# Performance work log

Measured on AMD Instinct MI355X. Metric: run time of the kernel, lower is better.

## Reference

```python
import jax, jax.numpy as jnp
import numpy as np

B, S, D, H, HD, MEM = 2, 2048, 1024, 16, 64, 512
SPARSITY_Q = 0.1


def setup_inputs() -> dict:
    key = jax.random.key(0)
    ks = jax.random.split(key, 12)
    s = 1.0 / np.sqrt(D).astype(np.float32)
    return {
        "hidden_states": jax.random.normal(ks[0], (B, S, D), jnp.float32),
        "attention_mask": jnp.ones((B, S), jnp.int32),
        "past_k": jax.random.normal(ks[1], (B, H, MEM, HD), jnp.float32),
        "past_v": jax.random.normal(ks[2], (B, H, MEM, HD), jnp.float32),
        "Wq": jax.random.normal(ks[3], (D, D), jnp.float32) * s,
        "bq": jnp.zeros((D,), jnp.float32),
        "Wk": jax.random.normal(ks[4], (D, D), jnp.float32) * s,
        "bk": jnp.zeros((D,), jnp.float32),
        "Wv": jax.random.normal(ks[5], (D, D), jnp.float32) * s,
        "bv": jnp.zeros((D,), jnp.float32),
        "Wo": jax.random.normal(ks[6], (D, D), jnp.float32) * s,
        "bo": jnp.zeros((D,), jnp.float32),
    }


def reference(hidden_states, attention_mask, past_k, past_v,
              Wq, bq, Wk, bk, Wv, bv, Wo, bo):
    b, s, d = hidden_states.shape
    # projections -> [b, h, s, hd]
    def split_heads(x):
        return x.reshape(b, s, H, HD).transpose(0, 2, 1, 3)
    q = split_heads(hidden_states @ Wq + bq)
    k = split_heads(hidden_states @ Wk + bk)
    v = split_heads(hidden_states @ Wv + bv)
    # concat KV cache along key length
    k = jnp.concatenate([past_k, k], axis=2)  # [b, h, mem+s, hd]
    v = jnp.concatenate([past_v, v], axis=2)
    past_len = past_k.shape[2]
    mask = jnp.concatenate(
        [jnp.ones((b, past_len), attention_mask.dtype), attention_mask], axis=1)
    scale = 1.0 / float(np.sqrt(HD))
    scores = jnp.einsum("bhqd,bhkd->bhqk", q, k) * scale  # [b,h,s,mem+s]
    # per-row quantile threshold sparsification (torch.quantile, linear interp)
    thr = jnp.quantile(scores, SPARSITY_Q, axis=-1, keepdims=True)
    neg_inf = jnp.float32(-jnp.inf)
    scores = jnp.where(scores < thr, neg_inf, scores)
    scores = jnp.where(mask[:, None, None, :] == 0, neg_inf, scores)
    attn = jax.nn.softmax(scores, axis=-1)  # dropout is identity in eval
    out = jnp.einsum("bhqk,bhkd->bhqd", attn, v)
    out = out.transpose(0, 2, 1, 3).reshape(b, s, d) @ Wo + bo
    new_k = k[:, :, -MEM:, :]
    new_v = v[:, :, -MEM:, :]
    return out, (new_k, new_v)
```

## Files before the change

### kernel.cpp

```cpp
#include <hip/hip_runtime.h>
#include <stdint.h>

typedef unsigned short ushort_t;
typedef __attribute__((ext_vector_type(8))) short bf16x8;
typedef __attribute__((ext_vector_type(4))) float f32x4;

#define BB 2
#define SS 2048
#define DD 1024
#define HH 16
#define HDD 64
#define MEMM 512
#define KTOT 2560
#define NKB 80
#define NROWS (BB*HH*SS)


__device__ __forceinline__ float bf2f(uint32_t u) {
    return __uint_as_float(u << 16);
}
__device__ __forceinline__ ushort_t f2bf(float f) {
    uint32_t u = __float_as_uint(f);
    uint32_t r = (u + 0x7FFFu + ((u >> 16) & 1u)) >> 16;
    return (ushort_t)r;
}
__device__ __forceinline__ uint32_t mapkey(uint32_t u) {
    return (u & 0x8000u) ? (0xFFFFu ^ u) : (u | 0x8000u);
}
__device__ __forceinline__ uint32_t unmapkey(uint32_t k) {
    return (k & 0x8000u) ? (k ^ 0x8000u) : (0xFFFFu ^ k);
}

__global__ __launch_bounds__(256) void cast_hidden_kernel(
    const float* __restrict__ h, ushort_t* __restrict__ hb)
{
    size_t i0 = ((size_t)blockIdx.x * 256 + threadIdx.x) * 16;
    ushort_t o[16];
#pragma unroll
    for (int j = 0; j < 4; ++j) {
        float4 v = *(const float4*)&h[i0 + j * 4];
        o[j * 4 + 0] = f2bf(v.x); o[j * 4 + 1] = f2bf(v.y);
        o[j * 4 + 2] = f2bf(v.z); o[j * 4 + 3] = f2bf(v.w);
    }
    *(uint4*)&hb[i0] = *(uint4*)&o[0];
    *(uint4*)&hb[i0 + 8] = *(uint4*)&o[8];
}

__global__ __launch_bounds__(256) void transw_kernel(
    const float* __restrict__ Wq, const float* __restrict__ Wk,
    const float* __restrict__ Wv, const float* __restrict__ Wo,
    ushort_t* __restrict__ WtAll)
{
    __shared__ ushort_t T[64][66];
    const int z = blockIdx.z;
    const float* W = (z == 0) ? Wq : (z == 1) ? Wk : (z == 2) ? Wv : Wo;
    ushort_t* dst = WtAll + (size_t)z * DD * DD;
    const int k0 = blockIdx.x * 64, n0 = blockIdx.y * 64;
    const int t = threadIdx.x;
    const int kk = t >> 2, c4 = (t & 3) * 16;
#pragma unroll
    for (int j = 0; j < 4; ++j) {
        float4 v = *(const float4*)&W[(size_t)(k0 + kk) * DD + n0 + c4 + j * 4];
        T[kk][c4 + j * 4 + 0] = f2bf(v.x);
        T[kk][c4 + j * 4 + 1] = f2bf(v.y);
        T[kk][c4 + j * 4 + 2] = f2bf(v.z);
        T[kk][c4 + j * 4 + 3] = f2bf(v.w);
    }
    __syncthreads();
    const int nn = t >> 2, kc = (t & 3) * 16;
    ushort_t tmp[16];
#pragma unroll
    for (int j = 0; j < 16; ++j) tmp[j] = T[kc + j][nn];
    *(uint4*)&dst[(size_t)(n0 + nn) * DD + k0 + kc] = *(uint4*)&tmp[0];
    *(uint4*)&dst[(size_t)(n0 + nn) * DD + k0 + kc + 8] = *(uint4*)&tmp[8];
}

__global__ __launch_bounds__(256) void gemm128_kernel(
    const ushort_t* __restrict__ A, const ushort_t* __restrict__ Bt, int mode,
    const float* __restrict__ bq, const float* __restrict__ bk, const float* __restrict__ bv,
    float* __restrict__ outf,
    ushort_t* __restrict__ q_bf, ushort_t* __restrict__ kbf, ushort_t* __restrict__ vbf,
    float* __restrict__ nk, float* __restrict__ nv)
{
    __shared__ __align__(16) ushort_t As[128 * 32];
    __shared__ __align__(16) ushort_t Bs[128 * 32];
    const int tid = threadIdx.x;
    const int lane = tid & 63, w = tid >> 6;
    const int wm = w >> 1, wn = w & 1;
    const int row16 = lane & 15, quad = lane >> 4;
    const int n0 = blockIdx.x * 128, m0 = blockIdx.y * 128;

    const int r0 = tid >> 2, c0 = (tid & 3) * 8;
    const int r1 = (tid + 256) >> 2, c1 = ((tid + 256) & 3) * 8;

    f32x4 acc[4][4];
#pragma unroll
    for (int i = 0; i < 4; ++i)
#pragma unroll
        for (int j = 0; j < 4; ++j) acc[i][j] = (f32x4){0.f, 0.f, 0.f, 0.f};

    for (int k0 = 0; k0 < DD; k0 += 32) {
        *(uint4*)&As[tid * 8]         = *(const uint4*)&A [(size_t)(m0 + r0) * DD + k0 + c0];
        *(uint4*)&As[(tid + 256) * 8] = *(const uint4*)&A [(size_t)(m0 + r1) * DD + k0 + c1];
        *(uint4*)&Bs[tid * 8]         = *(const uint4*)&Bt[(size_t)(n0 + r0) * DD + k0 + c0];
        *(uint4*)&Bs[(tid + 256) * 8] = *(const uint4*)&Bt[(size_t)(n0 + r1) * DD + k0 + c1];
        __syncthreads();
        bf16x8 af[4], bfr[4];
#pragma unroll
        for (int mt = 0; mt < 4; ++mt)
            af[mt] = *(const bf16x8*)&As[(wm * 64 + mt * 16 + row16) * 32 + quad * 8];
#pragma unroll
        for (int nt = 0; nt < 4; ++nt)
            bfr[nt] = *(const bf16x8*)&Bs[(wn * 64 + nt * 16 + row16) * 32 + quad * 8];
#pragma unroll
        for (int mt = 0; mt < 4; ++mt)
#pragma unroll
            for (int nt = 0; nt < 4; ++nt)
                acc[mt][nt] = __builtin_amdgcn_mfma_f32_16x16x32_bf16(
                    af[mt], bfr[nt], acc[mt][nt], 0, 0, 0);
        __syncthreads();
    }

#pragma unroll
    for (int nt = 0; nt < 4; ++nt) {
        const int nb = n0 + wn * 64 + nt * 16;
        if (mode == 0) {
#pragma unroll
            for (int mt = 0; mt < 4; ++mt) {
#pragma unroll
                for (int r = 0; r < 4; ++r) {
                    int m = m0 + wm * 64 + mt * 16 + quad * 4 + r;
                    int n = nb + row16;
                    outf[(size_t)m * DD + n] = acc[mt][nt][r] + bq[n];
                }
            }
        } else {
            const int sel = nb >> 10;
            const float* bias = (sel == 0) ? bq : (sel == 1) ? bk : bv;
#pragma unroll
            for (int mt = 0; mt < 4; ++mt) {
#pragma unroll
                for (int r = 0; r < 4; ++r) {
                    int m = m0 + wm * 64 + mt * 16 + quad * 4 + r;
                    int nn = (nb + row16) & 1023;
                    float v = acc[mt][nt][r] + bias[nn];
                    int b = m >> 11, s = m & (SS - 1);
                    int h = nn >> 6, d = nn & 63;
                    size_t bh = (size_t)b * HH + h;
                    if (sel == 0) {
                        q_bf[(bh * SS + s) * HDD + d] = f2bf(v);
                    } else {
                        ushort_t* dst = (sel == 1) ? kbf : vbf;
                        dst[(bh * KTOT + MEMM + s) * HDD + d] = f2bf(v);
                        if (s >= SS - MEMM) {
                            float* nf = (sel == 1) ? nk : nv;
                            nf[(bh * MEMM + (s - (SS - MEMM))) * HDD + d] = v;
                        }
                    }
                }
            }
        }
    }
}

__global__ __launch_bounds__(256) void cast_past_kernel(
    const float* __restrict__ pk, const float* __restrict__ pv,
    ushort_t* __restrict__ kbf, ushort_t* __restrict__ vbf)
{
    int idx = blockIdx.x * 256 + threadIdx.x;
    int bh = idx >> 15;
    int rem = idx & 32767;
    size_t dst = (size_t)bh * KTOT * HDD + rem;
    kbf[dst] = f2bf(pk[idx]);
    vbf[dst] = f2bf(pv[idx]);
}

__global__ __launch_bounds__(256) void transpose_v_kernel(
    const ushort_t* __restrict__ vbf, ushort_t* __restrict__ vt)
{
    __shared__ ushort_t T[64][72];
    const int k0 = blockIdx.x * 64;
    const int bh = blockIdx.y;
    const int t = threadIdx.x;
    const int rr = t >> 3, cc = (t & 7) * 8;
#pragma unroll
    for (int p = 0; p < 2; ++p) {
        int kk = p * 32 + rr;
        *(uint4*)&T[kk][cc] =
            *(const uint4*)(vbf + ((size_t)bh * KTOT + k0 + kk) * HDD + cc);
    }
    __syncthreads();
    const int ld = t & 63, nt = t >> 6;
    const int sr = ld & 15, q = ld >> 4;
#pragma unroll
    for (int kbl = 0; kbl < 2; ++kbl) {
        ushort_t tmp[8];
#pragma unroll
        for (int j = 0; j < 8; ++j) tmp[j] = T[kbl * 32 + q * 8 + j][nt * 16 + sr];
        *(uint4*)(vt + (((size_t)bh * NKB + (k0 >> 5) + kbl) * 4 + nt) * 512 + ld * 8)
            = *(uint4*)tmp;
    }
}

__global__ __launch_bounds__(256) void score_kernel(
    const ushort_t* __restrict__ qbf, const ushort_t* __restrict__ kbf,
    ushort_t* __restrict__ sbuf, int bh0)
{
    __shared__ __align__(16) ushort_t Ts[64][264];
    const int w = threadIdx.x >> 6, lane = threadIdx.x & 63;
    const int kt = blockIdx.x, qt = blockIdx.y;
    const int lbh = blockIdx.z, bh = bh0 + lbh;
    const int m0 = qt * 64 + w * 16;
    const int row16 = lane & 15, quad = lane >> 4;

    const ushort_t* qrow = qbf + ((size_t)bh * SS + m0 + row16) * HDD + quad * 8;
    bf16x8 a0 = *(const bf16x8*)qrow;
    bf16x8 a1 = *(const bf16x8*)(qrow + 32);
    const ushort_t* kbase = kbf + ((size_t)bh * KTOT + kt * 256 + row16) * HDD + quad * 8;

    bf16x8 b0c = *(const bf16x8*)kbase;
    bf16x8 b1c = *(const bf16x8*)(kbase + 32);
#pragma unroll
    for (int nt = 0; nt < 16; ++nt) {
        bf16x8 b0n, b1n;
        if (nt < 15) {
            const ushort_t* kr = kbase + (size_t)(nt + 1) * 16 * HDD;
            b0n = *(const bf16x8*)kr;
            b1n = *(const bf16x8*)(kr + 32);
        }
        f32x4 acc = {0.f, 0.f, 0.f, 0.f};
        acc = __builtin_amdgcn_mfma_f32_16x16x32_bf16(a0, b0c, acc, 0, 0, 0);
        acc = __builtin_amdgcn_mfma_f32_16x16x32_bf16(a1, b1c, acc, 0, 0, 0);
#pragma unroll
        for (int r = 0; r < 4; ++r)
            Ts[w * 16 + quad * 4 + r][nt * 16 + row16] = f2bf(acc[r] * 0.125f);
        b0c = b0n; b1c = b1n;
    }
    const int pnl = lbh * (SS / 16) + qt * 4 + w;
    ushort_t* dstb = sbuf + ((size_t)pnl * NKB + kt * 8) * 512 + lane * 8;
    const int c0 = (lane >> 4) * 8;
    const int rs = w * 16 + (lane & 15);
#pragma unroll
    for (int kbl = 0; kbl < 8; ++kbl)
        *(uint4*)(dstb + kbl * 512) = *(const uint4*)&Ts[rs][kbl * 32 + c0];
}

__device__ __forceinline__ uint32_t wave_iscan(uint32_t x, int lane) {
#pragma unroll
    for (int d = 1; d < 64; d <<= 1) {
        uint32_t t = __shfl_up(x, d, 64);
        if (lane >= d) x += t;
    }
    return x;
}
__device__ __forceinline__ void select_from_counts(
    const uint32_t* c, uint32_t R, int lane, uint32_t* bin_out, uint32_t* rem_out)
{
    uint32_t s = c[0] + c[1] + c[2] + c[3];
    uint32_t incl = wave_iscan(s, lane);
    uint32_t excl = incl - s;
    uint64_t bal = __ballot(incl > R);
    int fl = __ffsll((unsigned long long)bal) - 1;
    uint32_t exf = __shfl(excl, fl, 64);
    uint32_t c0 = __shfl(c[0], fl, 64), c1 = __shfl(c[1], fl, 64);
    uint32_t c2 = __shfl(c[2], fl, 64), c3 = __shfl(c[3], fl, 64);
    uint32_t cc[4] = {c0, c1, c2, c3};
    uint32_t cum = exf, bin = fl * 4, rem = 0;
#pragma unroll
    for (int i = 0; i < 4; ++i) {
        if (cum + cc[i] > R) { bin = fl * 4 + i; rem = R - cum; break; }
        cum += cc[i];
    }
    *bin_out = bin;
    *rem_out = rem;
}

__device__ __forceinline__ uint32_t select768(
    const uint32_t* Hr, uint32_t T, int lane)
{
    uint32_t wd[6];
    uint32_t s = 0;
#pragma unroll
    for (int i = 0; i < 6; ++i) {
        wd[i] = Hr[lane * 6 + i];
        s += (wd[i] & 0xFFFFu) + (wd[i] >> 16);
    }
    uint32_t incl = wave_iscan(s, lane);
    uint32_t excl = incl - s;
    uint64_t bal = __ballot(incl > T);
    int fl = __ffsll((unsigned long long)bal) - 1;
    uint32_t cum = __shfl(excl, fl, 64);
    uint32_t wf[6];
#pragma unroll
    for (int i = 0; i < 6; ++i) wf[i] = __shfl(wd[i], fl, 64);
    uint32_t o = (uint32_t)fl * 12u;
#pragma unroll
    for (int i = 0; i < 12; ++i) {
        uint32_t cnt = (wf[i >> 1] >> ((i & 1) * 16)) & 0xFFFFu;
        if (cum + cnt > T) { o = (uint32_t)fl * 12u + (uint32_t)i; break; }
        cum += cnt;
    }
    return o;
}

__global__ __launch_bounds__(256, 4) void quant_kernel(
    const ushort_t* __restrict__ sbuf, float* __restrict__ thr_out, int bh0)
{
    __shared__ uint32_t H[16][385];
    __shared__ uint32_t cw[4][16];
    const int tid = threadIdx.x;
    const int w = tid >> 6, lane = tid & 63;
    const int sr = lane & 15;
    const int p = blockIdx.x;
    const size_t grow0 = (size_t)bh0 * SS + (size_t)p * 16;
    uint32_t* Hf = &H[0][0];

    for (int i = tid; i < 16 * 385; i += 256) Hf[i] = 0u;
    __syncthreads();

    const ushort_t* src = sbuf + ((size_t)p * NKB + w * 20) * 512 + lane * 8;
    uint32_t nBel = 0, nReg = 0;
    for (int c = 0; c < 20; ++c) {
        uint4 v = *(const uint4*)(src + (size_t)c * 512);
        uint32_t ww[4] = {v.x, v.y, v.z, v.w};
#pragma unroll
        for (int q = 0; q < 4; ++q) {
            uint32_t t0 = (ww[q] >> 8) & 255u, lo0 = ww[q] & 255u;
            uint32_t t1 = ww[q] >> 24,         lo1 = (ww[q] >> 16) & 255u;
            nBel += (t0 >= 0xC1u);
            nBel += (t1 >= 0xC1u);
            uint32_t cls0 = 0xC0u - t0;
            uint32_t cls1 = 0xC0u - t1;
            if (cls0 <= 2u) {
                ++nReg;
                uint32_t o = cls0 * 256u + (lo0 ^ 255u);
                atomicAdd(&H[sr][o >> 1], 1u << ((o & 1u) << 4));
            }
            if (cls1 <= 2u) {
                ++nReg;
                uint32_t o = cls1 * 256u + (lo1 ^ 255u);
                atomicAdd(&H[sr][o >> 1], 1u << ((o & 1u) << 4));
            }
        }
    }
    uint32_t pk = nBel | (nReg << 16);
    pk += (uint32_t)__shfl_xor(pk, 16, 64);
    pk += (uint32_t)__shfl_xor(pk, 32, 64);
    if (lane < 16) cw[w][lane] = pk;
    __syncthreads();

    for (int j = 0; j < 4; ++j) {
        const int rho = w * 4 + j;
        const uint32_t P = cw[0][rho] + cw[1][rho] + cw[2][rho] + cw[3][rho];
        const uint32_t C0 = P & 0xFFFFu;
        const uint32_t C3 = C0 + (P >> 16);
        if (!(C0 <= 255u && C3 > 256u)) continue;
        uint32_t o0 = select768(&H[rho][0], 255u - C0, lane);
        uint32_t o1 = select768(&H[rho][0], 256u - C0, lane);
        uint32_t rawA = ((0xC0u - (o0 >> 8)) << 8) | ((o0 & 255u) ^ 255u);
        uint32_t rawB = ((0xC0u - (o1 >> 8)) << 8) | ((o1 & 255u) ^ 255u);
        if (lane == 0) {
            float fA = bf2f(rawA), fB = bf2f(rawB);
            thr_out[grow0 + rho] = fA + 0.9f * (fB - fA);
        }
    }

    bool okl = false;
    if (lane < 16) {
        uint32_t P = cw[0][lane] + cw[1][lane] + cw[2][lane] + cw[3][lane];
        uint32_t C0 = P & 0xFFFFu, C3 = C0 + (P >> 16);
        okl = (C0 <= 255u) && (C3 > 256u);
    }
    uint32_t fail = (uint32_t)__ballot(lane < 16 && !okl) & 0xFFFFu;
    while (fail) {
        const int rho = __ffs(fail) - 1; fail &= fail - 1;
        uint4 Wf[5];
        if (w == 0) {
#pragma unroll
            for (int j5 = 0; j5 < 5; ++j5) {
                int s = lane + j5 * 64;
                int kb = s >> 2, q = s & 3;
                Wf[j5] = *(const uint4*)(sbuf + ((size_t)p * NKB + kb) * 512
                                         + (q * 16 + rho) * 8);
            }
        }
        uint32_t rawAB[2] = {0u, 0u};
        for (int t = 0; t < 2; ++t) {
            if (tid < 256) Hf[tid] = 0u;
            __syncthreads();
            if (w == 0) {
#pragma unroll
                for (int j5 = 0; j5 < 5; ++j5) {
                    uint32_t wwf[4] = {Wf[j5].x, Wf[j5].y, Wf[j5].z, Wf[j5].w};
#pragma unroll
                    for (int q = 0; q < 4; ++q) {
                        atomicAdd(&Hf[mapkey(wwf[q] & 0xFFFFu) >> 8], 1u);
                        atomicAdd(&Hf[mapkey(wwf[q] >> 16) >> 8], 1u);
                    }
                }
            }
            __syncthreads();
            uint32_t binM = 0, rem = 0;
            if (w == 0) {
                uint32_t c4[4];
#pragma unroll
                for (int i = 0; i < 4; ++i) c4[i] = Hf[lane * 4 + i];
                select_from_counts(c4, 255u + (uint32_t)t, lane, &binM, &rem);
            }
            __syncthreads();
            if (tid < 256) Hf[tid] = 0u;
            __syncthreads();
            if (w == 0) {
#pragma unroll
                for (int j5 = 0; j5 < 5; ++j5) {
                    uint32_t wwf[4] = {Wf[j5].x, Wf[j5].y, Wf[j5].z, Wf[j5].w};
#pragma unroll
                    for (int q = 0; q < 4; ++q) {
                        uint32_t m0k = mapkey(wwf[q] & 0xFFFFu);
                        uint32_t m1k = mapkey(wwf[q] >> 16);
                        if ((m0k >> 8) == binM) atomicAdd(&Hf[m0k & 255u], 1u);
                        if ((m1k >> 8) == binM) atomicAdd(&Hf[m1k & 255u], 1u);
                    }
                }
            }
            __syncthreads();
            if (w == 0) {
                uint32_t c4[4];
#pragma unroll
                for (int i = 0; i < 4; ++i) c4[i] = Hf[lane * 4 + i];
                uint32_t low, r2;
                select_from_counts(c4, rem, lane, &low, &r2);
                rawAB[t] = unmapkey((binM << 8) | low);
            }
            __syncthreads();
        }
        if (tid == 0) {
            float fA = bf2f(rawAB[0]), fB = bf2f(rawAB[1]);
            thr_out[grow0 + rho] = fA + 0.9f * (fB - fA);
        }
        __syncthreads();
    }
}

__global__ __launch_bounds__(1024) void pv_kernel(
    const ushort_t* __restrict__ sbuf, const ushort_t* __restrict__ vt,
    const float* __restrict__ thr_arr,
    const int* __restrict__ amask, ushort_t* __restrict__ attn_bf, int bh0)
{
    __shared__ float red[8][64][21];
    const int tid = threadIdx.x;
    const int lane = tid & 63, w = tid >> 6;
    const int wr = w & 3, wq = w >> 2;
    const int row16 = lane & 15, quad = lane >> 4;
    const int qt = blockIdx.x;
    const int lbh = blockIdx.y, bh = bh0 + lbh;
    const int b = bh >> 4, h = bh & 15;
    const int m0 = qt * 64 + wr * 16;
    const int kb0 = wq * (NKB / 4);
    const int kbe = kb0 + NKB / 4;

    const int pnl = lbh * (SS / 16) + qt * 4 + wr;
    const ushort_t* abase = sbuf + (size_t)pnl * NKB * 512 + lane * 8;
    const ushort_t* bbase = vt + (size_t)bh * NKB * 2048 + lane * 8;
    const float thr = thr_arr[(size_t)bh * SS + m0 + row16];
    const int* amq = amask + b * SS + quad * 8;

    const uint32_t ow = (row16 == 0) ? 0x3F803F80u : 0u;
    uint4 ov; ov.x = ow; ov.y = ow; ov.z = ow; ov.w = ow;
    bf16x8 onesf; *(uint4*)&onesf = ov;

    f32x4 acc[4];
#pragma unroll
    for (int i = 0; i < 4; ++i) acc[i] = (f32x4){0.f, 0.f, 0.f, 0.f};
    f32x4 acc5 = (f32x4){0.f, 0.f, 0.f, 0.f};

    uint4 a_nxt = *(const uint4*)(abase + (size_t)kb0 * 512);
    uint4 b_nxt[4];
#pragma unroll
    for (int nt = 0; nt < 4; ++nt)
        b_nxt[nt] = *(const uint4*)(bbase + (size_t)kb0 * 2048 + nt * 512);
    int4 m_nxt0 = {1, 1, 1, 1}, m_nxt1 = {1, 1, 1, 1};
    if (kb0 * 32 >= MEMM) {
        m_nxt0 = *(const int4*)(amq + kb0 * 32 - MEMM);
        m_nxt1 = *(const int4*)(amq + kb0 * 32 - MEMM + 4);
    }

    for (int kb = kb0; kb < kbe; ++kb) {
        uint4 a_cur = a_nxt;
        uint4 b_cur[4] = {b_nxt[0], b_nxt[1], b_nxt[2], b_nxt[3]};
        int4 mc0 = m_nxt0, mc1 = m_nxt1;
        const int kbn = kb + 1;
        if (kbn < kbe) {
            a_nxt = *(const uint4*)(abase + (size_t)kbn * 512);
#pragma unroll
            for (int nt = 0; nt < 4; ++nt)
                b_nxt[nt] = *(const uint4*)(bbase + (size_t)kbn * 2048 + nt * 512);
            const int kn = kbn * 32;
            if (kn >= MEMM) {
                m_nxt0 = *(const int4*)(amq + kn - MEMM);
                m_nxt1 = *(const int4*)(amq + kn - MEMM + 4);
            }
        }
        uint32_t u[8] = {a_cur.x & 0xFFFFu, a_cur.x >> 16, a_cur.y & 0xFFFFu, a_cur.y >> 16,
                         a_cur.z & 0xFFFFu, a_cur.z >> 16, a_cur.w & 0xFFFFu, a_cur.w >> 16};
        int mm[8] = {mc0.x, mc0.y, mc0.z, mc0.w, mc1.x, mc1.y, mc1.z, mc1.w};
        const bool masked = (kb * 32 >= MEMM);
        float wv[8];
#pragma unroll
        for (int j = 0; j < 8; ++j) {
            float s = bf2f(u[j]);
            bool keep = (s >= thr);
            if (masked) keep = keep && (mm[j] != 0);
            wv[j] = keep ? __expf(s) : 0.f;
        }
        uint4 aq;
        asm("v_cvt_pk_bf16_f32 %0, %1, %2" : "=v"(aq.x) : "v"(wv[0]), "v"(wv[1]));
        asm("v_cvt_pk_bf16_f32 %0, %1, %2" : "=v"(aq.y) : "v"(wv[2]), "v"(wv[3]));
        asm("v_cvt_pk_bf16_f32 %0, %1, %2" : "=v"(aq.z) : "v"(wv[4]), "v"(wv[5]));
        asm("v_cvt_pk_bf16_f32 %0, %1, %2" : "=v"(aq.w) : "v"(wv[6]), "v"(wv[7]));
        bf16x8 af;
        *(uint4*)&af = aq;
#pragma unroll
        for (int nt = 0; nt < 4; ++nt) {
            bf16x8 bf;
            *(uint4*)&bf = b_cur[nt];
            acc[nt] = __builtin_amdgcn_mfma_f32_16x16x32_bf16(af, bf, acc[nt], 0, 0, 0);
        }
        acc5 = __builtin_amdgcn_mfma_f32_16x16x32_bf16(af, onesf, acc5, 0, 0, 0);
    }

    if (w >= 8) {
        float* dst = &red[w - 8][lane][0];
#pragma unroll
        for (int nt = 0; nt < 4; ++nt)
#pragma unroll
            for (int r = 0; r < 4; ++r) dst[nt * 4 + r] = acc[nt][r];
#pragma unroll
        for (int r = 0; r < 4; ++r) dst[16 + r] = acc5[r];
    }
    __syncthreads();
    if (w < 8) {
        const float* s = &red[w][lane][0];
#pragma unroll
        for (int nt = 0; nt < 4; ++nt)
#pragma unroll
            for (int r = 0; r < 4; ++r) acc[nt][r] += s[nt * 4 + r];
#pragma unroll
        for (int r = 0; r < 4; ++r) acc5[r] += s[16 + r];
    }
    __syncthreads();
    if (w >= 4 && w < 8) {
        float* dst = &red[w - 4][lane][0];
#pragma unroll
        for (int nt = 0; nt < 4; ++nt)
#pragma unroll
            for (int r = 0; r < 4; ++r) dst[nt * 4 + r] = acc[nt][r];
#pragma unroll
        for (int r = 0; r < 4; ++r) dst[16 + r] = acc5[r];
    }
    __syncthreads();
    if (w < 4) {
        const float* s = &red[w][lane][0];
#pragma unroll
        for (int nt = 0; nt < 4; ++nt)
#pragma unroll
            for (int r = 0; r < 4; ++r) acc[nt][r] += s[nt * 4 + r];
#pragma unroll
        for (int r = 0; r < 4; ++r) acc5[r] += s[16 + r];

        float rinv[4];
#pragma unroll
        for (int r = 0; r < 4; ++r) {
            float rs = __shfl(acc5[r], quad * 16, 64);
            rinv[r] = 1.0f / rs;
        }
#pragma unroll
        for (int nt = 0; nt < 4; ++nt) {
#pragma unroll
            for (int r = 0; r < 4; ++r) {
                int row = quad * 4 + r;
                float val = acc[nt][r] * rinv[r];
                attn_bf[((size_t)b * SS + m0 + row) * DD + h * HDD + nt * 16 + row16] = f2bf(val);
            }
        }
    }
}

extern "C" void kernel_launch(void* const* d_in, const int* in_sizes, int n_in,
                              void* d_out, int out_size, void* d_ws, size_t ws_size,
                              hipStream_t stream)
{
    const float* hidden = (const float*)d_in[0];
    const int*   amask  = (const int*)d_in[1];
    const float* past_k = (const float*)d_in[2];
    const float* past_v = (const float*)d_in[3];
    const float* Wq = (const float*)d_in[4];
    const float* bq = (const float*)d_in[5];
    const float* Wk = (const float*)d_in[6];
    const float* bk = (const float*)d_in[7];
    const float* Wv = (const float*)d_in[8];
    const float* bv = (const float*)d_in[9];
    const float* Wo = (const float*)d_in[10];
    const float* bo = (const float*)d_in[11];

    float* out    = (float*)d_out;
    float* nk_out = out + (size_t)BB * SS * DD;
    float* nv_out = nk_out + (size_t)BB * HH * MEMM * HDD;

    char* base = (char*)d_ws;
    size_t off = 0;
    auto alloc = [&](size_t bytes) {
        char* p = base + off;
        off += (bytes + 255) & ~(size_t)255;
        return p;
    };
    ushort_t* hb    = (ushort_t*)alloc((size_t)BB * SS * DD * 2);
    ushort_t* WtAll = (ushort_t*)alloc((size_t)4 * DD * DD * 2);
    ushort_t* q_bf  = (ushort_t*)alloc((size_t)BB * HH * SS * HDD * 2);
    ushort_t* kbf   = (ushort_t*)alloc((size_t)BB * HH * KTOT * HDD * 2);
    ushort_t* vbf   = (ushort_t*)alloc((size_t)BB * HH * KTOT * HDD * 2);
    ushort_t* vt    = (ushort_t*)alloc((size_t)BB * HH * NKB * 4 * 512 * 2);
    ushort_t* abf   = (ushort_t*)alloc((size_t)BB * SS * DD * 2);
    float* thr_arr  = (float*)alloc((size_t)NROWS * 4);
    size_t fixed = off;
    const size_t sbuf_full = (size_t)NROWS * KTOT * 2;
    int nchunks = 32;
    for (int c = 1; c <= 32; c <<= 1) {
        if (fixed + sbuf_full / c + 256 <= ws_size) { nchunks = c; break; }
    }
    ushort_t* sbuf = (ushort_t*)alloc(sbuf_full / nchunks);
    const int bhpc = (BB * HH) / nchunks;

    dim3 blk(256);

    cast_hidden_kernel<<<dim3(1024), blk, 0, stream>>>(hidden, hb);
    transw_kernel<<<dim3(16, 16, 4), blk, 0, stream>>>(Wq, Wk, Wv, Wo, WtAll);
    gemm128_kernel<<<dim3(24, 32), blk, 0, stream>>>(
        hb, WtAll, 1, bq, bk, bv, nullptr, q_bf, kbf, vbf, nk_out, nv_out);
    cast_past_kernel<<<dim3(4096), blk, 0, stream>>>(past_k, past_v, kbf, vbf);
    transpose_v_kernel<<<dim3(KTOT / 64, BB * HH), blk, 0, stream>>>(vbf, vt);

    for (int ci = 0; ci < nchunks; ++ci) {
        int bh0 = ci * bhpc;
        score_kernel<<<dim3(KTOT / 256, SS / 64, bhpc), blk, 0, stream>>>(q_bf, kbf, sbuf, bh0);
        quant_kernel<<<dim3(bhpc * (SS / 16)), blk, 0, stream>>>(sbuf, thr_arr, bh0);
        pv_kernel<<<dim3(SS / 64, bhpc), dim3(1024), 0, stream>>>(sbuf, vt, thr_arr,
                                                                  amask, abf, bh0);
    }
    gemm128_kernel<<<dim3(8, 32), blk, 0, stream>>>(
        abf, WtAll + (size_t)3 * DD * DD, 0, bo, nullptr, nullptr, out,
        nullptr, nullptr, nullptr, nullptr, nullptr);
}
```

Before: 567.8 us.

## Fuse score, quantile threshold and PV into one LDS-resident attention kernel

Replaces the chunked three-kernel pipeline (score to global sbuf, quantile, PV) with a single kernel per 16-row panel. That kernel computes the bf16 scores into a 80KB LDS tile, builds the histogram quantile in place, and runs PV directly from shared memory. This removes the global write and double read of the full score matrix and the per-chunk launches. Block IDs are remapped so that heads stay grouped per XCD. In exchange, the large LDS footprint limits occupancy to about one block per CU, and PV drops from 16 waves to 4 per panel.

Result: slower. 828.5 us (+45.9%).

```diff
diff --git a/kernel.cpp b/kernel.cpp
--- a/kernel.cpp
+++ b/kernel.cpp
@@ -13,7 +13,7 @@
 #define MEMM 512
 #define KTOT 2560
 #define NKB 80
-#define NROWS (BB*HH*SS)
+#define NTILE 160
 
 
 __device__ __forceinline__ float bf2f(uint32_t u) {
@@ -202,49 +202,6 @@
     }
 }
 
-__global__ __launch_bounds__(256) void score_kernel(
-    const ushort_t* __restrict__ qbf, const ushort_t* __restrict__ kbf,
-    ushort_t* __restrict__ sbuf, int bh0)
-{
-    __shared__ __align__(16) ushort_t Ts[64][264];
-    const int w = threadIdx.x >> 6, lane = threadIdx.x & 63;
-    const int kt = blockIdx.x, qt = blockIdx.y;
-    const int lbh = blockIdx.z, bh = bh0 + lbh;
-    const int m0 = qt * 64 + w * 16;
-    const int row16 = lane & 15, quad = lane >> 4;
-
-    const ushort_t* qrow = qbf + ((size_t)bh * SS + m0 + row16) * HDD + quad * 8;
-    bf16x8 a0 = *(const bf16x8*)qrow;
-    bf16x8 a1 = *(const bf16x8*)(qrow + 32);
-    const ushort_t* kbase = kbf + ((size_t)bh * KTOT + kt * 256 + row16) * HDD + quad * 8;
-
-    bf16x8 b0c = *(const bf16x8*)kbase;
-    bf16x8 b1c = *(const bf16x8*)(kbase + 32);
-#pragma unroll
-    for (int nt = 0; nt < 16; ++nt) {
-        bf16x8 b0n, b1n;
-        if (nt < 15) {
-            const ushort_t* kr = kbase + (size_t)(nt + 1) * 16 * HDD;
-            b0n = *(const bf16x8*)kr;
-            b1n = *(const bf16x8*)(kr + 32);
-        }
-        f32x4 acc = {0.f, 0.f, 0.f, 0.f};
-        acc = __builtin_amdgcn_mfma_f32_16x16x32_bf16(a0, b0c, acc, 0, 0, 0);
-        acc = __builtin_amdgcn_mfma_f32_16x16x32_bf16(a1, b1c, acc, 0, 0, 0);
-#pragma unroll
-        for (int r = 0; r < 4; ++r)
-            Ts[w * 16 + quad * 4 + r][nt * 16 + row16] = f2bf(acc[r] * 0.125f);
-        b0c = b0n; b1c = b1n;
-    }
-    const int pnl = lbh * (SS / 16) + qt * 4 + w;
-    ushort_t* dstb = sbuf + ((size_t)pnl * NKB + kt * 8) * 512 + lane * 8;
-    const int c0 = (lane >> 4) * 8;
-    const int rs = w * 16 + (lane & 15);
-#pragma unroll
-    for (int kbl = 0; kbl < 8; ++kbl)
-        *(uint4*)(dstb + kbl * 512) = *(const uint4*)&Ts[rs][kbl * 32 + c0];
-}
-
 __device__ __forceinline__ uint32_t wave_iscan(uint32_t x, int lane) {
 #pragma unroll
     for (int d = 1; d < 64; d <<= 1) {
@@ -303,28 +260,72 @@
     return o;
 }
 
-__global__ __launch_bounds__(256, 4) void quant_kernel(
-    const ushort_t* __restrict__ sbuf, float* __restrict__ thr_out, int bh0)
-{
+__global__ __launch_bounds__(256) void fused_attn_kernel(
+    const ushort_t* __restrict__ qbf, const ushort_t* __restrict__ kbf,
+    const ushort_t* __restrict__ vt, const int* __restrict__ amask,
+    ushort_t* __restrict__ attn_bf)
+{
+    __shared__ __align__(16) ushort_t S[NTILE * 256];
     __shared__ uint32_t H[16][385];
     __shared__ uint32_t cw[4][16];
+    __shared__ float red[2][64][21];
+    __shared__ float thrs[16];
+    __shared__ uint32_t fb[2];
+
     const int tid = threadIdx.x;
     const int w = tid >> 6, lane = tid & 63;
-    const int sr = lane & 15;
-    const int p = blockIdx.x;
-    const size_t grow0 = (size_t)bh0 * SS + (size_t)p * 16;
-    uint32_t* Hf = &H[0][0];
-
-    for (int i = tid; i < 16 * 385; i += 256) Hf[i] = 0u;
-    __syncthreads();
-
-    const ushort_t* src = sbuf + ((size_t)p * NKB + w * 20) * 512 + lane * 8;
+    const int row16 = lane & 15, quad = lane >> 4;
+    const int bid = blockIdx.x;
+    const int xcd = bid & 7, slot = bid >> 3;
+    const int bh = xcd * 4 + (slot >> 7);
+    const int pnl = slot & 127;
+    const int b = bh >> 4, h = bh & 15;
+    const int m0 = pnl * 16;
+
+    const ushort_t* qrow = qbf + ((size_t)bh * SS + m0 + row16) * HDD + quad * 8;
+    bf16x8 q0 = *(const bf16x8*)qrow;
+    bf16x8 q1 = *(const bf16x8*)(qrow + 32);
+    const ushort_t* kbase = kbf + ((size_t)bh * KTOT + w * 640 + row16) * HDD + quad * 8;
+
+    uint4 rka[4], rkb[4];
+#pragma unroll
+    for (int i = 0; i < 4; ++i) {
+        rka[i] = *(const uint4*)(kbase + (size_t)i * 16 * HDD);
+        rkb[i] = *(const uint4*)(kbase + (size_t)i * 16 * HDD + 32);
+    }
+    for (int ii = 0; ii < 40; ii += 4) {
+#pragma unroll
+        for (int j = 0; j < 4; ++j) {
+            const int i = ii + j;
+            bf16x8 af0, af1;
+            *(uint4*)&af0 = rka[j];
+            *(uint4*)&af1 = rkb[j];
+            if (i + 4 < 40) {
+                rka[j] = *(const uint4*)(kbase + (size_t)(i + 4) * 16 * HDD);
+                rkb[j] = *(const uint4*)(kbase + (size_t)(i + 4) * 16 * HDD + 32);
+            }
+            f32x4 acc = {0.f, 0.f, 0.f, 0.f};
+            acc = __builtin_amdgcn_mfma_f32_16x16x32_bf16(af0, q0, acc, 0, 0, 0);
+            acc = __builtin_amdgcn_mfma_f32_16x16x32_bf16(af1, q1, acc, 0, 0, 0);
+            uint32_t p0, p1;
+            float s0 = acc[0] * 0.125f, s1 = acc[1] * 0.125f;
+            float s2 = acc[2] * 0.125f, s3 = acc[3] * 0.125f;
+            asm("v_cvt_pk_bf16_f32 %0, %1, %2" : "=v"(p0) : "v"(s0), "v"(s1));
+            asm("v_cvt_pk_bf16_f32 %0, %1, %2" : "=v"(p1) : "v"(s2), "v"(s3));
+            uint2 pp; pp.x = p0; pp.y = p1;
+            *(uint2*)&S[(w * 40 + i) * 256 + lane * 4] = pp;
+        }
+    }
+
+    for (int i = tid; i < 16 * 385; i += 256) (&H[0][0])[i] = 0u;
+    __syncthreads();
+
     uint32_t nBel = 0, nReg = 0;
-    for (int c = 0; c < 20; ++c) {
-        uint4 v = *(const uint4*)(src + (size_t)c * 512);
-        uint32_t ww[4] = {v.x, v.y, v.z, v.w};
-#pragma unroll
-        for (int q = 0; q < 4; ++q) {
+    for (int i = 0; i < 40; ++i) {
+        uint2 v = *(const uint2*)&S[(w * 40 + i) * 256 + lane * 4];
+        uint32_t ww[2] = {v.x, v.y};
+#pragma unroll
+        for (int q = 0; q < 2; ++q) {
             uint32_t t0 = (ww[q] >> 8) & 255u, lo0 = ww[q] & 255u;
             uint32_t t1 = ww[q] >> 24,         lo1 = (ww[q] >> 16) & 255u;
             nBel += (t0 >= 0xC1u);
@@ -334,136 +335,95 @@
             if (cls0 <= 2u) {
                 ++nReg;
                 uint32_t o = cls0 * 256u + (lo0 ^ 255u);
-                atomicAdd(&H[sr][o >> 1], 1u << ((o & 1u) << 4));
+                atomicAdd(&H[row16][o >> 1], 1u << ((o & 1u) << 4));
             }
             if (cls1 <= 2u) {
                 ++nReg;
                 uint32_t o = cls1 * 256u + (lo1 ^ 255u);
-                atomicAdd(&H[sr][o >> 1], 1u << ((o & 1u) << 4));
-            }
-        }
-    }
-    uint32_t pk = nBel | (nReg << 16);
-    pk += (uint32_t)__shfl_xor(pk, 16, 64);
-    pk += (uint32_t)__shfl_xor(pk, 32, 64);
-    if (lane < 16) cw[w][lane] = pk;
+                atomicAdd(&H[row16][o >> 1], 1u << ((o & 1u) << 4));
+            }
+        }
+    }
+    uint32_t pk2 = nBel | (nReg << 16);
+    pk2 += (uint32_t)__shfl_xor(pk2, 16, 64);
+    pk2 += (uint32_t)__shfl_xor(pk2, 32, 64);
+    if (lane < 16) cw[w][lane] = pk2;
     __syncthreads();
 
     for (int j = 0; j < 4; ++j) {
         const int rho = w * 4 + j;
         const uint32_t P = cw[0][rho] + cw[1][rho] + cw[2][rho] + cw[3][rho];
-        const uint32_t C0 = P & 0xFFFFu;
-        const uint32_t C3 = C0 + (P >> 16);
-        if (!(C0 <= 255u && C3 > 256u)) continue;
-        uint32_t o0 = select768(&H[rho][0], 255u - C0, lane);
-        uint32_t o1 = select768(&H[rho][0], 256u - C0, lane);
+        const uint32_t c0v = P & 0xFFFFu;
+        const uint32_t c3v = c0v + (P >> 16);
+        if (!(c0v <= 255u && c3v > 256u)) continue;
+        uint32_t o0 = select768(&H[rho][0], 255u - c0v, lane);
+        uint32_t o1 = select768(&H[rho][0], 256u - c0v, lane);
         uint32_t rawA = ((0xC0u - (o0 >> 8)) << 8) | ((o0 & 255u) ^ 255u);
         uint32_t rawB = ((0xC0u - (o1 >> 8)) << 8) | ((o1 & 255u) ^ 255u);
-        if (lane == 0) {
-            float fA = bf2f(rawA), fB = bf2f(rawB);
-            thr_out[grow0 + rho] = fA + 0.9f * (fB - fA);
-        }
+        if (lane == 0)
+            thrs[rho] = bf2f(rawA) + 0.9f * (bf2f(rawB) - bf2f(rawA));
     }
 
     bool okl = false;
     if (lane < 16) {
         uint32_t P = cw[0][lane] + cw[1][lane] + cw[2][lane] + cw[3][lane];
-        uint32_t C0 = P & 0xFFFFu, C3 = C0 + (P >> 16);
-        okl = (C0 <= 255u) && (C3 > 256u);
+        uint32_t c0v = P & 0xFFFFu, c3v = c0v + (P >> 16);
+        okl = (c0v <= 255u) && (c3v > 256u);
     }
     uint32_t fail = (uint32_t)__ballot(lane < 16 && !okl) & 0xFFFFu;
+    uint32_t* Hf = &H[0][0];
     while (fail) {
         const int rho = __ffs(fail) - 1; fail &= fail - 1;
-        uint4 Wf[5];
-        if (w == 0) {
-#pragma unroll
-            for (int j5 = 0; j5 < 5; ++j5) {
-                int s = lane + j5 * 64;
-                int kb = s >> 2, q = s & 3;
-                Wf[j5] = *(const uint4*)(sbuf + ((size_t)p * NKB + kb) * 512
-                                         + (q * 16 + rho) * 8);
-            }
-        }
         uint32_t rawAB[2] = {0u, 0u};
-        for (int t = 0; t < 2; ++t) {
-            if (tid < 256) Hf[tid] = 0u;
+#pragma unroll
+        for (int t2 = 0; t2 < 2; ++t2) {
             __syncthreads();
-            if (w == 0) {
-#pragma unroll
-                for (int j5 = 0; j5 < 5; ++j5) {
-                    uint32_t wwf[4] = {Wf[j5].x, Wf[j5].y, Wf[j5].z, Wf[j5].w};
-#pragma unroll
-                    for (int q = 0; q < 4; ++q) {
-                        atomicAdd(&Hf[mapkey(wwf[q] & 0xFFFFu) >> 8], 1u);
-                        atomicAdd(&Hf[mapkey(wwf[q] >> 16) >> 8], 1u);
-                    }
-                }
-            }
+            for (int i = tid; i < 257; i += 256) Hf[i] = 0u;
             __syncthreads();
-            uint32_t binM = 0, rem = 0;
-            if (w == 0) {
-                uint32_t c4[4];
-#pragma unroll
-                for (int i = 0; i < 4; ++i) c4[i] = Hf[lane * 4 + i];
-                select_from_counts(c4, 255u + (uint32_t)t, lane, &binM, &rem);
-            }
-            __syncthreads();
-            if (tid < 256) Hf[tid] = 0u;
-            __syncthreads();
-            if (w == 0) {
-#pragma unroll
-                for (int j5 = 0; j5 < 5; ++j5) {
-                    uint32_t wwf[4] = {Wf[j5].x, Wf[j5].y, Wf[j5].z, Wf[j5].w};
-#pragma unroll
-                    for (int q = 0; q < 4; ++q) {
-                        uint32_t m0k = mapkey(wwf[q] & 0xFFFFu);
-                        uint32_t m1k = mapkey(wwf[q] >> 16);
-                        if ((m0k >> 8) == binM) atomicAdd(&Hf[m0k & 255u], 1u);
-                        if ((m1k >> 8) == binM) atomicAdd(&Hf[m1k & 255u], 1u);
-                    }
-                }
+            for (int k = tid; k < KTOT; k += 256) {
+                uint32_t val = S[(k >> 4) * 256 + (((k & 15) >> 2) * 16 + rho) * 4 + (k & 3)];
+                atomicAdd(&Hf[mapkey(val) >> 8], 1u);
             }
             __syncthreads();
             if (w == 0) {
                 uint32_t c4[4];
 #pragma unroll
                 for (int i = 0; i < 4; ++i) c4[i] = Hf[lane * 4 + i];
+                uint32_t binM, rem;
+                select_from_counts(c4, 255u + (uint32_t)t2, lane, &binM, &rem);
+                if (lane == 0) { fb[0] = binM; fb[1] = rem; }
+            }
+            __syncthreads();
+            const uint32_t binM = fb[0], rem = fb[1];
+            for (int i = tid; i < 257; i += 256) Hf[i] = 0u;
+            __syncthreads();
+            for (int k = tid; k < KTOT; k += 256) {
+                uint32_t val = S[(k >> 4) * 256 + (((k & 15) >> 2) * 16 + rho) * 4 + (k & 3)];
+                uint32_t mk = mapkey(val);
+                if ((mk >> 8) == binM) atomicAdd(&Hf[mk & 255u], 1u);
+            }
+            __syncthreads();
+            if (w == 0) {
+                uint32_t c4[4];
+#pragma unroll
+                for (int i = 0; i < 4; ++i) c4[i] = Hf[lane * 4 + i];
                 uint32_t low, r2;
                 select_from_counts(c4, rem, lane, &low, &r2);
-                rawAB[t] = unmapkey((binM << 8) | low);
-            }
-            __syncthreads();
-        }
+                rawAB[t2] = unmapkey((binM << 8) | low);
+            }
+        }
+        __syncthreads();
         if (tid == 0) {
             float fA = bf2f(rawAB[0]), fB = bf2f(rawAB[1]);
-            thr_out[grow0 + rho] = fA + 0.9f * (fB - fA);
+            thrs[rho] = fA + 0.9f * (fB - fA);
         }
         __syncthreads();
     }
-}
-
-__global__ __launch_bounds__(1024) void pv_kernel(
-    const ushort_t* __restrict__ sbuf, const ushort_t* __restrict__ vt,
-    const float* __restrict__ thr_arr,
-    const int* __restrict__ amask, ushort_t* __restrict__ attn_bf, int bh0)
-{
-    __shared__ float red[8][64][21];
-    const int tid = threadIdx.x;
-    const int lane = tid & 63, w = tid >> 6;
-    const int wr = w & 3, wq = w >> 2;
-    const int row16 = lane & 15, quad = lane >> 4;
-    const int qt = blockIdx.x;
-    const int lbh = blockIdx.y, bh = bh0 + lbh;
-    const int b = bh >> 4, h = bh & 15;
-    const int m0 = qt * 64 + wr * 16;
-    const int kb0 = wq * (NKB / 4);
-    const int kbe = kb0 + NKB / 4;
-
-    const int pnl = lbh * (SS / 16) + qt * 4 + wr;
-    const ushort_t* abase = sbuf + (size_t)pnl * NKB * 512 + lane * 8;
+    __syncthreads();
+
+    const float thr = thrs[row16];
+    const int* amq = amask + b * SS + quad * 8;
     const ushort_t* bbase = vt + (size_t)bh * NKB * 2048 + lane * 8;
-    const float thr = thr_arr[(size_t)bh * SS + m0 + row16];
-    const int* amq = amask + b * SS + quad * 8;
 
     const uint32_t ow = (row16 == 0) ? 0x3F803F80u : 0u;
     uint4 ov; ov.x = ow; ov.y = ow; ov.z = ow; ov.w = ow;
@@ -474,7 +434,10 @@
     for (int i = 0; i < 4; ++i) acc[i] = (f32x4){0.f, 0.f, 0.f, 0.f};
     f32x4 acc5 = (f32x4){0.f, 0.f, 0.f, 0.f};
 
-    uint4 a_nxt = *(const uint4*)(abase + (size_t)kb0 * 512);
+    const int kb0 = w * 20, kbe = kb0 + 20;
+    const int sA = ((quad & 1) * 32 + row16) * 4;
+    const int sB = sA + 64;
+
     uint4 b_nxt[4];
 #pragma unroll
     for (int nt = 0; nt < 4; ++nt)
@@ -486,12 +449,10 @@
     }
 
     for (int kb = kb0; kb < kbe; ++kb) {
-        uint4 a_cur = a_nxt;
         uint4 b_cur[4] = {b_nxt[0], b_nxt[1], b_nxt[2], b_nxt[3]};
         int4 mc0 = m_nxt0, mc1 = m_nxt1;
         const int kbn = kb + 1;
         if (kbn < kbe) {
-            a_nxt = *(const uint4*)(abase + (size_t)kbn * 512);
 #pragma unroll
             for (int nt = 0; nt < 4; ++nt)
                 b_nxt[nt] = *(const uint4*)(bbase + (size_t)kbn * 2048 + nt * 512);
@@ -501,8 +462,11 @@
                 m_nxt1 = *(const int4*)(amq + kn - MEMM + 4);
             }
         }
-        uint32_t u[8] = {a_cur.x & 0xFFFFu, a_cur.x >> 16, a_cur.y & 0xFFFFu, a_cur.y >> 16,
-                         a_cur.z & 0xFFFFu, a_cur.z >> 16, a_cur.w & 0xFFFFu, a_cur.w >> 16};
+        const int tS = (2 * kb + (quad >> 1)) * 256;
+        uint2 g0 = *(const uint2*)&S[tS + sA];
+        uint2 g1 = *(const uint2*)&S[tS + sB];
+        uint32_t u[8] = {g0.x & 0xFFFFu, g0.x >> 16, g0.y & 0xFFFFu, g0.y >> 16,
+                         g1.x & 0xFFFFu, g1.x >> 16, g1.y & 0xFFFFu, g1.y >> 16};
         int mm[8] = {mc0.x, mc0.y, mc0.z, mc0.w, mc1.x, mc1.y, mc1.z, mc1.w};
         const bool masked = (kb * 32 >= MEMM);
         float wv[8];
@@ -529,8 +493,8 @@
         acc5 = __builtin_amdgcn_mfma_f32_16x16x32_bf16(af, onesf, acc5, 0, 0, 0);
     }
 
-    if (w >= 8) {
-        float* dst = &red[w - 8][lane][0];
+    if (w >= 2) {
+        float* dst = &red[w - 2][lane][0];
 #pragma unroll
         for (int nt = 0; nt < 4; ++nt)
 #pragma unroll
@@ -539,7 +503,7 @@
         for (int r = 0; r < 4; ++r) dst[16 + r] = acc5[r];
     }
     __syncthreads();
-    if (w < 8) {
+    if (w < 2) {
         const float* s = &red[w][lane][0];
 #pragma unroll
         for (int nt = 0; nt < 4; ++nt)
@@ -549,8 +513,8 @@
         for (int r = 0; r < 4; ++r) acc5[r] += s[16 + r];
     }
     __syncthreads();
-    if (w >= 4 && w < 8) {
-        float* dst = &red[w - 4][lane][0];
+    if (w == 1) {
+        float* dst = &red[0][lane][0];
 #pragma unroll
         for (int nt = 0; nt < 4; ++nt)
 #pragma unroll
@@ -559,8 +523,8 @@
         for (int r = 0; r < 4; ++r) dst[16 + r] = acc5[r];
     }
     __syncthreads();
-    if (w < 4) {
-        const float* s = &red[w][lane][0];
+    if (w == 0) {
+        const float* s = &red[0][lane][0];
 #pragma unroll
         for (int nt = 0; nt < 4; ++nt)
 #pragma unroll
@@ -621,15 +585,6 @@
     ushort_t* vbf   = (ushort_t*)alloc((size_t)BB * HH * KTOT * HDD * 2);
     ushort_t* vt    = (ushort_t*)alloc((size_t)BB * HH * NKB * 4 * 512 * 2);
     ushort_t* abf   = (ushort_t*)alloc((size_t)BB * SS * DD * 2);
-    float* thr_arr  = (float*)alloc((size_t)NROWS * 4);
-    size_t fixed = off;
-    const size_t sbuf_full = (size_t)NROWS * KTOT * 2;
-    int nchunks = 32;
-    for (int c = 1; c <= 32; c <<= 1) {
-        if (fixed + sbuf_full / c + 256 <= ws_size) { nchunks = c; break; }
-    }
-    ushort_t* sbuf = (ushort_t*)alloc(sbuf_full / nchunks);
-    const int bhpc = (BB * HH) / nchunks;
 
     dim3 blk(256);
 
@@ -640,13 +595,9 @@
     cast_past_kernel<<<dim3(4096), blk, 0, stream>>>(past_k, past_v, kbf, vbf);
     transpose_v_kernel<<<dim3(KTOT / 64, BB * HH), blk, 0, stream>>>(vbf, vt);
 
-    for (int ci = 0; ci < nchunks; ++ci) {
-        int bh0 = ci * bhpc;
-        score_kernel<<<dim3(KTOT / 256, SS / 64, bhpc), blk, 0, stream>>>(q_bf, kbf, sbuf, bh0);
-        quant_kernel<<<dim3(bhpc * (SS / 16)), blk, 0, stream>>>(sbuf, thr_arr, bh0);
-        pv_kernel<<<dim3(SS / 64, bhpc), dim3(1024), 0, stream>>>(sbuf, vt, thr_arr,
-                                                                  amask, abf, bh0);
-    }
+    fused_attn_kernel<<<dim3(BB * HH * (SS / 16)), blk, 0, stream>>>(
+        q_bf, kbf, vt, amask, abf);
+
     gemm128_kernel<<<dim3(8, 32), blk, 0, stream>>>(
         abf, WtAll + (size_t)3 * DD * DD, 0, bo, nullptr, nullptr, out,
         nullptr, nullptr, nullptr, nullptr, nullptr);
```
